# Kernel tuning notes

Measured on AMD Instinct MI355X. Metric: run time of the kernel, lower is better.

Reference implementation:

```python
import jax, jax.numpy as jnp
import numpy as np

B, T, D, UNITS = 64, 2048, 512, 512


def setup_inputs() -> dict:
    key = jax.random.key(0)
    ks = jax.random.split(key, 6)
    scale = 1.0 / np.sqrt(D)
    return {
        "features": jax.random.normal(ks[0], (B, T, D), dtype=jnp.float32),
        "hidden": jax.random.normal(ks[1], (B, D), dtype=jnp.float32),
        "W1_w": jax.random.normal(ks[2], (D, UNITS), dtype=jnp.float32) * scale,
        "W1_b": jnp.zeros((UNITS,), dtype=jnp.float32),
        "W2_w": jax.random.normal(ks[3], (D, UNITS), dtype=jnp.float32) * scale,
        "W2_b": jnp.zeros((UNITS,), dtype=jnp.float32),
        "V_w": jax.random.normal(ks[4], (UNITS, 1), dtype=jnp.float32) * (1.0 / np.sqrt(UNITS)),
        "V_b": jnp.zeros((1,), dtype=jnp.float32),
    }


def reference(features, hidden, W1_w, W1_b, W2_w, W2_b, V_w, V_b):
    # features: [B, T, D], hidden: [B, D]
    f_proj = jnp.einsum("btd,du->btu", features, W1_w) + W1_b      # [B, T, U]
    h_proj = (hidden @ W2_w + W2_b)[:, None, :]                     # [B, 1, U]
    score = jnp.tanh(f_proj + h_proj) @ V_w + V_b                   # [B, T, 1]
    attn = jax.nn.softmax(score, axis=1)                            # softmax over time
    context = jnp.sum(attn * features, axis=1)                      # [B, D]
    return context
```

## Files before the change

kernel.cpp:

```cpp
#include <hip/hip_runtime.h>
#include <hip/hip_bf16.h>

#define B_DIM 64
#define T_DIM 2048
#define D_DIM 512
#define U_DIM 512

typedef __bf16 bf16x8 __attribute__((ext_vector_type(8)));
typedef float  f32x4  __attribute__((ext_vector_type(4)));
typedef unsigned int u32;

__device__ __forceinline__ void gl_lds16(const __bf16* g, __bf16* l) {
    __builtin_amdgcn_global_load_lds(
        (const __attribute__((address_space(1))) u32*)g,
        (__attribute__((address_space(3))) u32*)l,
        16, 0, 0);
}

__global__ void w1s_kernel(const float* __restrict__ W1w, __bf16* __restrict__ w1s) {
    __shared__ float tile[64][33];
    const int tid = threadIdx.x;
    const int kb2 = blockIdx.x;
    const int ub  = blockIdx.y;
    #pragma unroll
    for (int i = 0; i < 8; ++i) {
        int k = i * 4 + (tid >> 6);
        int u = tid & 63;
        tile[u][k] = W1w[(kb2 * 32 + k) * U_DIM + ub * 64 + u];
    }
    __syncthreads();
    int u_l = tid >> 2;
    int kp  = (tid & 3) * 8;
    bf16x8 w;
    #pragma unroll
    for (int j = 0; j < 8; ++j) w[j] = (__bf16)tile[u_l][kp + j];
    *reinterpret_cast<bf16x8*>(&w1s[kb2 * 16384 + (ub * 64 + u_l) * 32 + kp]) = w;
}

__global__ void hproj_kernel(const float* __restrict__ hidden,
                             const float* __restrict__ W2w,
                             const float* __restrict__ W2b,
                             const float* __restrict__ W1b,
                             float* __restrict__ hp) {
    int b = blockIdx.x;
    int u = blockIdx.y * 256 + threadIdx.x;
    float acc = W2b[u] + W1b[u];
    const float* hrow = hidden + b * D_DIM;
    #pragma unroll 8
    for (int d = 0; d < D_DIM; ++d)
        acc = fmaf(hrow[d], W2w[d * U_DIM + u], acc);
    hp[b * U_DIM + u] = acc;
}

__global__ __launch_bounds__(256, 2) void score_kernel(
        const float*  __restrict__ features,
        const __bf16* __restrict__ w1s,
        const float*  __restrict__ hp,
        const float*  __restrict__ Vw,
        float*        __restrict__ scores) {
    __shared__ __align__(16) __bf16 As0[64 * 32];
    __shared__ __align__(16) __bf16 As1[64 * 32];
    __shared__ __align__(16) __bf16 Bs0[512 * 32];
    __shared__ __align__(16) __bf16 Bs1[512 * 32];
    __shared__ float red[4 * 64];

    const int tid  = threadIdx.x;
    const int row0 = blockIdx.x * 64;
    const int b    = row0 >> 11;

    const int wn   = tid >> 6;
    const int lane = tid & 63;
    const int l16  = lane & 15;
    const int quad = lane >> 4;

    const int arow = tid >> 2;
    const int aq   = tid & 3;

    f32x4 acc[4][8];
    #pragma unroll
    for (int i = 0; i < 4; ++i)
        #pragma unroll
        for (int j = 0; j < 8; ++j)
            acc[i][j] = (f32x4)0.0f;

    const float* ag = features + (size_t)(row0 + arow) * D_DIM + aq * 8;

    for (int ko = 0; ko < 8; ++ko) {
        const __bf16* bsrc0 = w1s + (2 * ko) * 16384 + tid * 8;
        const __bf16* bsrc1 = w1s + (2 * ko + 1) * 16384 + tid * 8;
        #pragma unroll
        for (int c = 0; c < 8; ++c) {
            gl_lds16(bsrc0 + c * 2048, Bs0 + c * 2048 + tid * 8);
            gl_lds16(bsrc1 + c * 2048, Bs1 + c * 2048 + tid * 8);
        }
        {
            const float4* s0 = reinterpret_cast<const float4*>(ag + ko * 64);
            const float4* s1 = reinterpret_cast<const float4*>(ag + ko * 64 + 32);
            float4 v0 = s0[0], v1 = s0[1];
            float4 v2 = s1[0], v3 = s1[1];
            bf16x8 w0, w1;
            w0[0] = (__bf16)v0.x; w0[1] = (__bf16)v0.y; w0[2] = (__bf16)v0.z; w0[3] = (__bf16)v0.w;
            w0[4] = (__bf16)v1.x; w0[5] = (__bf16)v1.y; w0[6] = (__bf16)v1.z; w0[7] = (__bf16)v1.w;
            w1[0] = (__bf16)v2.x; w1[1] = (__bf16)v2.y; w1[2] = (__bf16)v2.z; w1[3] = (__bf16)v2.w;
            w1[4] = (__bf16)v3.x; w1[5] = (__bf16)v3.y; w1[6] = (__bf16)v3.z; w1[7] = (__bf16)v3.w;
            *reinterpret_cast<bf16x8*>(&As0[arow * 32 + aq * 8]) = w0;
            *reinterpret_cast<bf16x8*>(&As1[arow * 32 + aq * 8]) = w1;
        }
        __syncthreads();

        #pragma unroll
        for (int ks = 0; ks < 2; ++ks) {
            const __bf16* Ap = ks ? As1 : As0;
            const __bf16* Bp = ks ? Bs1 : Bs0;
            bf16x8 af[4], bfr[8];
            #pragma unroll
            for (int mt = 0; mt < 4; ++mt)
                af[mt] = *reinterpret_cast<const bf16x8*>(
                    &Ap[(mt * 16 + l16) * 32 + quad * 8]);
            #pragma unroll
            for (int nt = 0; nt < 8; ++nt)
                bfr[nt] = *reinterpret_cast<const bf16x8*>(
                    &Bp[(wn * 128 + nt * 16 + l16) * 32 + quad * 8]);
            #pragma unroll
            for (int mt = 0; mt < 4; ++mt)
                #pragma unroll
                for (int nt = 0; nt < 8; ++nt)
                    acc[mt][nt] = __builtin_amdgcn_mfma_f32_16x16x32_bf16(
                        af[mt], bfr[nt], acc[mt][nt], 0, 0, 0);
        }
        __syncthreads();
    }

    float hpv[8], vwv[8];
    #pragma unroll
    for (int nt = 0; nt < 8; ++nt) {
        int u = wn * 128 + nt * 16 + l16;
        hpv[nt] = hp[b * U_DIM + u];
        vwv[nt] = Vw[u];
    }
    #pragma unroll
    for (int mt = 0; mt < 4; ++mt) {
        #pragma unroll
        for (int reg = 0; reg < 4; ++reg) {
            float s = 0.0f;
            #pragma unroll
            for (int nt = 0; nt < 8; ++nt) {
                float x = acc[mt][nt][reg] + hpv[nt];
                float e = exp2f(x * 2.88539008f);
                float th = 1.0f - 2.0f * __builtin_amdgcn_rcpf(e + 1.0f);
                s = fmaf(th, vwv[nt], s);
            }
            s += __shfl_xor(s, 1);
            s += __shfl_xor(s, 2);
            s += __shfl_xor(s, 4);
            s += __shfl_xor(s, 8);
            if (l16 == 0)
                red[wn * 64 + mt * 16 + quad * 4 + reg] = s;
        }
    }
    __syncthreads();
    if (tid < 64)
        scores[row0 + tid] = red[tid] + red[64 + tid] + red[128 + tid] + red[192 + tid];
}

__global__ void softmax_kernel(const float* __restrict__ scores, float* __restrict__ attn) {
    int b = blockIdx.x;
    int tid = threadIdx.x;
    __shared__ float red[4], red2[4];

    float s[8];
    float m = -1e30f;
    #pragma unroll
    for (int i = 0; i < 8; ++i) {
        s[i] = scores[b * T_DIM + i * 256 + tid];
        m = fmaxf(m, s[i]);
    }
    #pragma unroll
    for (int off = 1; off < 64; off <<= 1) m = fmaxf(m, __shfl_xor(m, off));
    if ((tid & 63) == 0) red[tid >> 6] = m;
    __syncthreads();
    m = fmaxf(fmaxf(red[0], red[1]), fmaxf(red[2], red[3]));

    float e[8], sum = 0.0f;
    #pragma unroll
    for (int i = 0; i < 8; ++i) {
        e[i] = exp2f((s[i] - m) * 1.44269504f);
        sum += e[i];
    }
    #pragma unroll
    for (int off = 1; off < 64; off <<= 1) sum += __shfl_xor(sum, off);
    if ((tid & 63) == 0) red2[tid >> 6] = sum;
    __syncthreads();
    sum = red2[0] + red2[1] + red2[2] + red2[3];
    float inv = 1.0f / sum;
    #pragma unroll
    for (int i = 0; i < 8; ++i)
        attn[b * T_DIM + i * 256 + tid] = e[i] * inv;
}

__global__ void context_kernel(const float* __restrict__ attn,
                               const float* __restrict__ features,
                               float* __restrict__ out) {
    __shared__ float4 red[256];
    const int tid = threadIdx.x;
    const int b   = blockIdx.y;
    const int d4  = (blockIdx.x << 5) + (tid & 31);
    const int tp  = tid >> 5;

    const float4* f  = reinterpret_cast<const float4*>(features) + (size_t)b * T_DIM * 128;
    const float*  ar = attn + b * T_DIM;

    float4 acc = {0.f, 0.f, 0.f, 0.f};
    #pragma unroll 8
    for (int i = 0; i < 256; ++i) {
        int t = tp * 256 + i;
        float a = ar[t];
        float4 v = f[(size_t)t * 128 + d4];
        acc.x = fmaf(a, v.x, acc.x);
        acc.y = fmaf(a, v.y, acc.y);
        acc.z = fmaf(a, v.z, acc.z);
        acc.w = fmaf(a, v.w, acc.w);
    }
    red[tid] = acc;
    __syncthreads();
    if (tp == 0) {
        float4 s = red[tid];
        #pragma unroll
        for (int j = 1; j < 8; ++j) {
            float4 v = red[tid + 32 * j];
            s.x += v.x; s.y += v.y; s.z += v.z; s.w += v.w;
        }
        reinterpret_cast<float4*>(out)[b * 128 + d4] = s;
    }
}

extern "C" void kernel_launch(void* const* d_in, const int* in_sizes, int n_in,
                              void* d_out, int out_size, void* d_ws, size_t ws_size,
                              hipStream_t stream) {
    const float* features = (const float*)d_in[0];
    const float* hidden   = (const float*)d_in[1];
    const float* W1w      = (const float*)d_in[2];
    const float* W1b      = (const float*)d_in[3];
    const float* W2w      = (const float*)d_in[4];
    const float* W2b      = (const float*)d_in[5];
    const float* Vw       = (const float*)d_in[6];

    char* ws = (char*)d_ws;
    __bf16* w1s    = (__bf16*)ws;
    float*  scores = (float*)(ws + (512u << 10));
    float*  attn   = (float*)(ws + (1024u << 10));
    float*  hp     = (float*)(ws + (1536u << 10));

    hipLaunchKernelGGL(w1s_kernel, dim3(16, 8), dim3(256), 0, stream, W1w, w1s);
    hipLaunchKernelGGL(hproj_kernel, dim3(B_DIM, 2), dim3(256), 0, stream,
                       hidden, W2w, W2b, W1b, hp);
    hipLaunchKernelGGL(score_kernel, dim3(2048), dim3(256), 0, stream,
                       features, w1s, hp, Vw, scores);
    hipLaunchKernelGGL(softmax_kernel, dim3(B_DIM), dim3(256), 0, stream, scores, attn);
    hipLaunchKernelGGL(context_kernel, dim3(4, B_DIM), dim3(256), 0, stream,
                       attn, features, (float*)d_out);
}
```

Measured before the change: 491.8 us.

## Stage full A tile in LDS once and stream W1 fragments from global into registers

The score kernel now converts the block's whole 64x512 features tile to bf16 into shared memory once, up front, instead of per k-step. The W1 operand is no longer staged through LDS; each wave loads its MFMA B fragments straight from global memory into registers, double-buffered with a prefetch of the next k-plane. This removes the per-iteration barriers and the LDS traffic for W1. In exchange it raises register pressure, performs uncoalesced-ish global fragment loads with each wave relying on cache for W1 reuse, and keeps LDS at a similar size.

After: 514.1 us. 1.05x slower.

```diff
diff --git a/kernel.cpp b/kernel.cpp
--- a/kernel.cpp
+++ b/kernel.cpp
@@ -9,13 +9,6 @@
 typedef __bf16 bf16x8 __attribute__((ext_vector_type(8)));
 typedef float  f32x4  __attribute__((ext_vector_type(4)));
 typedef unsigned int u32;
-
-__device__ __forceinline__ void gl_lds16(const __bf16* g, __bf16* l) {
-    __builtin_amdgcn_global_load_lds(
-        (const __attribute__((address_space(1))) u32*)g,
-        (__attribute__((address_space(3))) u32*)l,
-        16, 0, 0);
-}
 
 __global__ void w1s_kernel(const float* __restrict__ W1w, __bf16* __restrict__ w1s) {
     __shared__ float tile[64][33];
@@ -58,10 +51,7 @@
         const float*  __restrict__ hp,
         const float*  __restrict__ Vw,
         float*        __restrict__ scores) {
-    __shared__ __align__(16) __bf16 As0[64 * 32];
-    __shared__ __align__(16) __bf16 As1[64 * 32];
-    __shared__ __align__(16) __bf16 Bs0[512 * 32];
-    __shared__ __align__(16) __bf16 Bs1[512 * 32];
+    __shared__ __align__(16) __bf16 As[16 * 64 * 32];
     __shared__ float red[4 * 64];
 
     const int tid  = threadIdx.x;
@@ -73,9 +63,6 @@
     const int l16  = lane & 15;
     const int quad = lane >> 4;
 
-    const int arow = tid >> 2;
-    const int aq   = tid & 3;
-
     f32x4 acc[4][8];
     #pragma unroll
     for (int i = 0; i < 4; ++i)
@@ -83,53 +70,59 @@
         for (int j = 0; j < 8; ++j)
             acc[i][j] = (f32x4)0.0f;
 
-    const float* ag = features + (size_t)(row0 + arow) * D_DIM + aq * 8;
-
-    for (int ko = 0; ko < 8; ++ko) {
-        const __bf16* bsrc0 = w1s + (2 * ko) * 16384 + tid * 8;
-        const __bf16* bsrc1 = w1s + (2 * ko + 1) * 16384 + tid * 8;
-        #pragma unroll
-        for (int c = 0; c < 8; ++c) {
-            gl_lds16(bsrc0 + c * 2048, Bs0 + c * 2048 + tid * 8);
-            gl_lds16(bsrc1 + c * 2048, Bs1 + c * 2048 + tid * 8);
+    {
+        const int arow = tid >> 2;
+        const int aq   = tid & 3;
+        const float* ag = features + (size_t)(row0 + arow) * D_DIM + aq * 8;
+        __bf16* aw = As + arow * 32 + aq * 8;
+        #pragma unroll
+        for (int c = 0; c < 16; ++c) {
+            const float4* s = reinterpret_cast<const float4*>(ag + c * 32);
+            float4 v0 = s[0], v1 = s[1];
+            bf16x8 w;
+            w[0] = (__bf16)v0.x; w[1] = (__bf16)v0.y; w[2] = (__bf16)v0.z; w[3] = (__bf16)v0.w;
+            w[4] = (__bf16)v1.x; w[5] = (__bf16)v1.y; w[6] = (__bf16)v1.z; w[7] = (__bf16)v1.w;
+            *reinterpret_cast<bf16x8*>(aw + c * 2048) = w;
         }
-        {
-            const float4* s0 = reinterpret_cast<const float4*>(ag + ko * 64);
-            const float4* s1 = reinterpret_cast<const float4*>(ag + ko * 64 + 32);
-            float4 v0 = s0[0], v1 = s0[1];
-            float4 v2 = s1[0], v3 = s1[1];
-            bf16x8 w0, w1;
-            w0[0] = (__bf16)v0.x; w0[1] = (__bf16)v0.y; w0[2] = (__bf16)v0.z; w0[3] = (__bf16)v0.w;
-            w0[4] = (__bf16)v1.x; w0[5] = (__bf16)v1.y; w0[6] = (__bf16)v1.z; w0[7] = (__bf16)v1.w;
-            w1[0] = (__bf16)v2.x; w1[1] = (__bf16)v2.y; w1[2] = (__bf16)v2.z; w1[3] = (__bf16)v2.w;
-            w1[4] = (__bf16)v3.x; w1[5] = (__bf16)v3.y; w1[6] = (__bf16)v3.z; w1[7] = (__bf16)v3.w;
-            *reinterpret_cast<bf16x8*>(&As0[arow * 32 + aq * 8]) = w0;
-            *reinterpret_cast<bf16x8*>(&As1[arow * 32 + aq * 8]) = w1;
-        }
-        __syncthreads();
-
-        #pragma unroll
-        for (int ks = 0; ks < 2; ++ks) {
-            const __bf16* Ap = ks ? As1 : As0;
-            const __bf16* Bp = ks ? Bs1 : Bs0;
-            bf16x8 af[4], bfr[8];
-            #pragma unroll
-            for (int mt = 0; mt < 4; ++mt)
-                af[mt] = *reinterpret_cast<const bf16x8*>(
-                    &Ap[(mt * 16 + l16) * 32 + quad * 8]);
-            #pragma unroll
-            for (int nt = 0; nt < 8; ++nt)
-                bfr[nt] = *reinterpret_cast<const bf16x8*>(
-                    &Bp[(wn * 128 + nt * 16 + l16) * 32 + quad * 8]);
-            #pragma unroll
-            for (int mt = 0; mt < 4; ++mt)
-                #pragma unroll
-                for (int nt = 0; nt < 8; ++nt)
-                    acc[mt][nt] = __builtin_amdgcn_mfma_f32_16x16x32_bf16(
-                        af[mt], bfr[nt], acc[mt][nt], 0, 0, 0);
-        }
-        __syncthreads();
-    }
+    }
+
+    const __bf16* bb = w1s + (wn * 128 + l16) * 32 + quad * 8;
+    const __bf16* Ab = As + l16 * 32 + quad * 8;
+
+    bf16x8 bA[8], bB[8];
+    #pragma unroll
+    for (int nt = 0; nt < 8; ++nt)
+        bA[nt] = *reinterpret_cast<const bf16x8*>(bb + nt * 512);
+
+    __syncthreads();
+
+#define PLANE_STEP(KB, BC, BN, PF)                                           \
+    {                                                                        \
+        if (PF) {                                                            \
+            _Pragma("unroll")                                                \
+            for (int nt = 0; nt < 8; ++nt)                                   \
+                BN[nt] = *reinterpret_cast<const bf16x8*>(                   \
+                    bb + ((KB) + 1) * 16384 + nt * 512);                     \
+        }                                                                    \
+        bf16x8 af[4];                                                        \
+        _Pragma("unroll")                                                    \
+        for (int mt = 0; mt < 4; ++mt)                                       \
+            af[mt] = *reinterpret_cast<const bf16x8*>(                       \
+                Ab + (KB) * 2048 + mt * 512);                                \
+        _Pragma("unroll")                                                    \
+        for (int mt = 0; mt < 4; ++mt)                                       \
+            _Pragma("unroll")                                                \
+            for (int nt = 0; nt < 8; ++nt)                                   \
+                acc[mt][nt] = __builtin_amdgcn_mfma_f32_16x16x32_bf16(       \
+                    af[mt], BC[nt], acc[mt][nt], 0, 0, 0);                   \
+    }
+
+    #pragma unroll
+    for (int k2 = 0; k2 < 8; ++k2) {
+        PLANE_STEP(2 * k2,     bA, bB, 1);
+        PLANE_STEP(2 * k2 + 1, bB, bA, ((2 * k2 + 1) < 15));
+    }
+#undef PLANE_STEP
 
     float hpv[8], vwv[8];
     #pragma unroll
```

## Fuse softmax and context into score kernel with split-softmax combine

Applied to the files above, without the earlier changes.

The score kernel now computes a per-chunk local softmax (max and sum) and a partial weighted context over its 64 rows, writing partials that a small combine kernel rescales and reduces. This removes the separate softmax pass and the second full read of features in the context kernel, since features are re-read right after the GEMM while likely still cache-resident. The GEMM loop is also restructured into a 16-step double-buffered pipeline that prefetches the next K slice while computing the current one. In exchange it writes 4 MB of partial contexts and adds a combine pass; the LDS footprint stays similar.

Measured after the change: 475.8 us. 3.3% less time.

```diff
diff --git a/kernel.cpp b/kernel.cpp
--- a/kernel.cpp
+++ b/kernel.cpp
@@ -52,20 +52,24 @@
     hp[b * U_DIM + u] = acc;
 }
 
-__global__ __launch_bounds__(256, 2) void score_kernel(
+__global__ __launch_bounds__(256, 2) void score_ctx_kernel(
         const float*  __restrict__ features,
         const __bf16* __restrict__ w1s,
         const float*  __restrict__ hp,
         const float*  __restrict__ Vw,
-        float*        __restrict__ scores) {
-    __shared__ __align__(16) __bf16 As0[64 * 32];
-    __shared__ __align__(16) __bf16 As1[64 * 32];
-    __shared__ __align__(16) __bf16 Bs0[512 * 32];
-    __shared__ __align__(16) __bf16 Bs1[512 * 32];
-    __shared__ float red[4 * 64];
+        float*        __restrict__ ctx,
+        float*        __restrict__ mv,
+        float*        __restrict__ lv) {
+    __shared__ __align__(16) char smem[8192 + 65536 + 1024 + 256];
+    __bf16* As  = (__bf16*)smem;
+    __bf16* Bs  = (__bf16*)(smem + 8192);
+    float*  red = (float*)(smem + 8192 + 65536);
+    float*  se  = (float*)(smem + 8192 + 65536 + 1024);
+    float4* red4 = (float4*)Bs;
 
     const int tid  = threadIdx.x;
-    const int row0 = blockIdx.x * 64;
+    const int chunk = blockIdx.x;
+    const int row0 = chunk * 64;
     const int b    = row0 >> 11;
 
     const int wn   = tid >> 6;
@@ -73,61 +77,65 @@
     const int l16  = lane & 15;
     const int quad = lane >> 4;
 
+    f32x4 acc[4][8];
+    #pragma unroll
+    for (int i = 0; i < 4; ++i)
+        #pragma unroll
+        for (int j = 0; j < 8; ++j)
+            acc[i][j] = (f32x4)0.0f;
+
     const int arow = tid >> 2;
     const int aq   = tid & 3;
-
-    f32x4 acc[4][8];
-    #pragma unroll
-    for (int i = 0; i < 4; ++i)
-        #pragma unroll
-        for (int j = 0; j < 8; ++j)
-            acc[i][j] = (f32x4)0.0f;
-
-    const float* ag = features + (size_t)(row0 + arow) * D_DIM + aq * 8;
-
-    for (int ko = 0; ko < 8; ++ko) {
-        const __bf16* bsrc0 = w1s + (2 * ko) * 16384 + tid * 8;
-        const __bf16* bsrc1 = w1s + (2 * ko + 1) * 16384 + tid * 8;
-        #pragma unroll
-        for (int c = 0; c < 8; ++c) {
-            gl_lds16(bsrc0 + c * 2048, Bs0 + c * 2048 + tid * 8);
-            gl_lds16(bsrc1 + c * 2048, Bs1 + c * 2048 + tid * 8);
-        }
-        {
-            const float4* s0 = reinterpret_cast<const float4*>(ag + ko * 64);
-            const float4* s1 = reinterpret_cast<const float4*>(ag + ko * 64 + 32);
-            float4 v0 = s0[0], v1 = s0[1];
-            float4 v2 = s1[0], v3 = s1[1];
-            bf16x8 w0, w1;
-            w0[0] = (__bf16)v0.x; w0[1] = (__bf16)v0.y; w0[2] = (__bf16)v0.z; w0[3] = (__bf16)v0.w;
-            w0[4] = (__bf16)v1.x; w0[5] = (__bf16)v1.y; w0[6] = (__bf16)v1.z; w0[7] = (__bf16)v1.w;
-            w1[0] = (__bf16)v2.x; w1[1] = (__bf16)v2.y; w1[2] = (__bf16)v2.z; w1[3] = (__bf16)v2.w;
-            w1[4] = (__bf16)v3.x; w1[5] = (__bf16)v3.y; w1[6] = (__bf16)v3.z; w1[7] = (__bf16)v3.w;
-            *reinterpret_cast<bf16x8*>(&As0[arow * 32 + aq * 8]) = w0;
-            *reinterpret_cast<bf16x8*>(&As1[arow * 32 + aq * 8]) = w1;
-        }
-        __syncthreads();
-
-        #pragma unroll
-        for (int ks = 0; ks < 2; ++ks) {
-            const __bf16* Ap = ks ? As1 : As0;
-            const __bf16* Bp = ks ? Bs1 : Bs0;
-            bf16x8 af[4], bfr[8];
+    const float* agp = features + (size_t)(row0 + arow) * D_DIM + aq * 8;
+
+    {
+        const __bf16* src = w1s + tid * 8;
+        #pragma unroll
+        for (int c = 0; c < 8; ++c)
+            gl_lds16(src + c * 2048, Bs + c * 2048 + tid * 8);
+        const float4* s = reinterpret_cast<const float4*>(agp);
+        float4 v0 = s[0], v1 = s[1];
+        bf16x8 w;
+        w[0] = (__bf16)v0.x; w[1] = (__bf16)v0.y; w[2] = (__bf16)v0.z; w[3] = (__bf16)v0.w;
+        w[4] = (__bf16)v1.x; w[5] = (__bf16)v1.y; w[6] = (__bf16)v1.z; w[7] = (__bf16)v1.w;
+        *reinterpret_cast<bf16x8*>(&As[arow * 32 + aq * 8]) = w;
+    }
+    __syncthreads();
+
+    #pragma unroll
+    for (int p = 0; p < 16; ++p) {
+        const int cur = p & 1;
+        if (p < 15) {
+            const int nxt = cur ^ 1;
+            const __bf16* src = w1s + (p + 1) * 16384 + tid * 8;
+            __bf16* dst = Bs + nxt * 16384 + tid * 8;
             #pragma unroll
-            for (int mt = 0; mt < 4; ++mt)
-                af[mt] = *reinterpret_cast<const bf16x8*>(
-                    &Ap[(mt * 16 + l16) * 32 + quad * 8]);
+            for (int c = 0; c < 8; ++c)
+                gl_lds16(src + c * 2048, dst + c * 2048);
+            const float4* s = reinterpret_cast<const float4*>(agp + (p + 1) * 32);
+            float4 v0 = s[0], v1 = s[1];
+            bf16x8 w;
+            w[0] = (__bf16)v0.x; w[1] = (__bf16)v0.y; w[2] = (__bf16)v0.z; w[3] = (__bf16)v0.w;
+            w[4] = (__bf16)v1.x; w[5] = (__bf16)v1.y; w[6] = (__bf16)v1.z; w[7] = (__bf16)v1.w;
+            *reinterpret_cast<bf16x8*>(&As[nxt * 2048 + arow * 32 + aq * 8]) = w;
+        }
+        const __bf16* Ap = As + cur * 2048;
+        const __bf16* Bp = Bs + cur * 16384;
+        bf16x8 af[4], bfr[8];
+        #pragma unroll
+        for (int mt = 0; mt < 4; ++mt)
+            af[mt] = *reinterpret_cast<const bf16x8*>(
+                &Ap[(mt * 16 + l16) * 32 + quad * 8]);
+        #pragma unroll
+        for (int nt = 0; nt < 8; ++nt)
+            bfr[nt] = *reinterpret_cast<const bf16x8*>(
+                &Bp[(wn * 128 + nt * 16 + l16) * 32 + quad * 8]);
+        #pragma unroll
+        for (int mt = 0; mt < 4; ++mt)
             #pragma unroll
             for (int nt = 0; nt < 8; ++nt)
-                bfr[nt] = *reinterpret_cast<const bf16x8*>(
-                    &Bp[(wn * 128 + nt * 16 + l16) * 32 + quad * 8]);
-            #pragma unroll
-            for (int mt = 0; mt < 4; ++mt)
-                #pragma unroll
-                for (int nt = 0; nt < 8; ++nt)
-                    acc[mt][nt] = __builtin_amdgcn_mfma_f32_16x16x32_bf16(
-                        af[mt], bfr[nt], acc[mt][nt], 0, 0, 0);
-        }
+                acc[mt][nt] = __builtin_amdgcn_mfma_f32_16x16x32_bf16(
+                    af[mt], bfr[nt], acc[mt][nt], 0, 0, 0);
         __syncthreads();
     }
 
@@ -159,78 +167,75 @@
         }
     }
     __syncthreads();
-    if (tid < 64)
-        scores[row0 + tid] = red[tid] + red[64 + tid] + red[128 + tid] + red[192 + tid];
-}
-
-__global__ void softmax_kernel(const float* __restrict__ scores, float* __restrict__ attn) {
-    int b = blockIdx.x;
-    int tid = threadIdx.x;
-    __shared__ float red[4], red2[4];
-
-    float s[8];
-    float m = -1e30f;
-    #pragma unroll
-    for (int i = 0; i < 8; ++i) {
-        s[i] = scores[b * T_DIM + i * 256 + tid];
-        m = fmaxf(m, s[i]);
-    }
-    #pragma unroll
-    for (int off = 1; off < 64; off <<= 1) m = fmaxf(m, __shfl_xor(m, off));
-    if ((tid & 63) == 0) red[tid >> 6] = m;
-    __syncthreads();
-    m = fmaxf(fmaxf(red[0], red[1]), fmaxf(red[2], red[3]));
-
-    float e[8], sum = 0.0f;
-    #pragma unroll
-    for (int i = 0; i < 8; ++i) {
-        e[i] = exp2f((s[i] - m) * 1.44269504f);
-        sum += e[i];
-    }
-    #pragma unroll
-    for (int off = 1; off < 64; off <<= 1) sum += __shfl_xor(sum, off);
-    if ((tid & 63) == 0) red2[tid >> 6] = sum;
-    __syncthreads();
-    sum = red2[0] + red2[1] + red2[2] + red2[3];
-    float inv = 1.0f / sum;
-    #pragma unroll
-    for (int i = 0; i < 8; ++i)
-        attn[b * T_DIM + i * 256 + tid] = e[i] * inv;
-}
-
-__global__ void context_kernel(const float* __restrict__ attn,
-                               const float* __restrict__ features,
+
+    if (tid < 64) {
+        float s = red[tid] + red[64 + tid] + red[128 + tid] + red[192 + tid];
+        float m = s;
+        #pragma unroll
+        for (int off = 1; off < 64; off <<= 1) m = fmaxf(m, __shfl_xor(m, off));
+        float e = exp2f((s - m) * 1.44269504f);
+        se[tid] = e;
+        float l = e;
+        #pragma unroll
+        for (int off = 1; off < 64; off <<= 1) l += __shfl_xor(l, off);
+        if (tid == 0) { mv[chunk] = m; lv[chunk] = l; }
+    }
+    __syncthreads();
+
+    {
+        const int col  = tid & 127;
+        const int half = tid >> 7;
+        const float4* fb = reinterpret_cast<const float4*>(features)
+                           + (size_t)row0 * 128 + col;
+        float4 a4 = {0.f, 0.f, 0.f, 0.f};
+        #pragma unroll 8
+        for (int i = 0; i < 32; ++i) {
+            int t = half * 32 + i;
+            float e = se[t];
+            float4 v = fb[(size_t)t * 128];
+            a4.x = fmaf(e, v.x, a4.x);
+            a4.y = fmaf(e, v.y, a4.y);
+            a4.z = fmaf(e, v.z, a4.z);
+            a4.w = fmaf(e, v.w, a4.w);
+        }
+        red4[tid] = a4;
+        __syncthreads();
+        if (half == 0) {
+            float4 v = red4[tid + 128];
+            a4 = red4[tid];
+            a4.x += v.x; a4.y += v.y; a4.z += v.z; a4.w += v.w;
+            reinterpret_cast<float4*>(ctx)[(size_t)chunk * 128 + col] = a4;
+        }
+    }
+}
+
+__global__ void combine_kernel(const float* __restrict__ ctx,
+                               const float* __restrict__ mv,
+                               const float* __restrict__ lv,
                                float* __restrict__ out) {
-    __shared__ float4 red[256];
+    __shared__ float w[32];
+    const int b   = blockIdx.x;
     const int tid = threadIdx.x;
-    const int b   = blockIdx.y;
-    const int d4  = (blockIdx.x << 5) + (tid & 31);
-    const int tp  = tid >> 5;
-
-    const float4* f  = reinterpret_cast<const float4*>(features) + (size_t)b * T_DIM * 128;
-    const float*  ar = attn + b * T_DIM;
-
-    float4 acc = {0.f, 0.f, 0.f, 0.f};
-    #pragma unroll 8
-    for (int i = 0; i < 256; ++i) {
-        int t = tp * 256 + i;
-        float a = ar[t];
-        float4 v = f[(size_t)t * 128 + d4];
-        acc.x = fmaf(a, v.x, acc.x);
-        acc.y = fmaf(a, v.y, acc.y);
-        acc.z = fmaf(a, v.z, acc.z);
-        acc.w = fmaf(a, v.w, acc.w);
-    }
-    red[tid] = acc;
-    __syncthreads();
-    if (tp == 0) {
-        float4 s = red[tid];
-        #pragma unroll
-        for (int j = 1; j < 8; ++j) {
-            float4 v = red[tid + 32 * j];
-            s.x += v.x; s.y += v.y; s.z += v.z; s.w += v.w;
-        }
-        reinterpret_cast<float4*>(out)[b * 128 + d4] = s;
+    if (tid < 32) {
+        float m = mv[b * 32 + tid];
+        float M = m;
+        #pragma unroll
+        for (int off = 1; off < 32; off <<= 1) M = fmaxf(M, __shfl_xor(M, off));
+        float wc = exp2f((m - M) * 1.44269504f);
+        float l  = lv[b * 32 + tid] * wc;
+        #pragma unroll
+        for (int off = 1; off < 32; off <<= 1) l += __shfl_xor(l, off);
+        w[tid] = wc / l;
+    }
+    __syncthreads();
+    #pragma unroll
+    for (int r = 0; r < 2; ++r) {
+        int d = r * 256 + tid;
+        float s = 0.0f;
+        #pragma unroll
+        for (int c = 0; c < 32; ++c)
+            s = fmaf(ctx[(size_t)(b * 32 + c) * 512 + d], w[c], s);
+        out[b * 512 + d] = s;
     }
 }
 
@@ -246,17 +251,17 @@
     const float* Vw       = (const float*)d_in[6];
 
     char* ws = (char*)d_ws;
-    __bf16* w1s    = (__bf16*)ws;
-    float*  scores = (float*)(ws + (512u << 10));
-    float*  attn   = (float*)(ws + (1024u << 10));
-    float*  hp     = (float*)(ws + (1536u << 10));
+    __bf16* w1s = (__bf16*)ws;
+    float*  hp  = (float*)(ws + (512u << 10));
+    float*  ctx = (float*)(ws + (640u << 10));
+    float*  mv  = (float*)(ws + (640u << 10) + (4u << 20));
+    float*  lv  = (float*)(ws + (640u << 10) + (4u << 20) + 8192u);
 
     hipLaunchKernelGGL(w1s_kernel, dim3(16, 8), dim3(256), 0, stream, W1w, w1s);
     hipLaunchKernelGGL(hproj_kernel, dim3(B_DIM, 2), dim3(256), 0, stream,
                        hidden, W2w, W2b, W1b, hp);
-    hipLaunchKernelGGL(score_kernel, dim3(2048), dim3(256), 0, stream,
-                       features, w1s, hp, Vw, scores);
-    hipLaunchKernelGGL(softmax_kernel, dim3(B_DIM), dim3(256), 0, stream, scores, attn);
-    hipLaunchKernelGGL(context_kernel, dim3(4, B_DIM), dim3(256), 0, stream,
-                       attn, features, (float*)d_out);
-}
+    hipLaunchKernelGGL(score_ctx_kernel, dim3(2048), dim3(256), 0, stream,
+                       features, w1s, hp, Vw, ctx, mv, lv);
+    hipLaunchKernelGGL(combine_kernel, dim3(B_DIM), dim3(256), 0, stream,
+                       ctx, mv, lv, (float*)d_out);
+}
```
